# Performance work log

Hardware: AMD Instinct MI355X
Metric: run time of the kernel (lower is better)

## Reference

```python
import jax, jax.numpy as jnp
import numpy as np

D_MODEL = 1024
NUM_HEADS = 16
HEAD_DIM = D_MODEL // NUM_HEADS
SCALE = HEAD_DIM ** -0.5


def setup_inputs() -> dict:
    key = jax.random.key(0)
    ks = jax.random.split(key, 9)
    B, T, D = 4, 2048, D_MODEL
    s = 1.0 / np.sqrt(D)
    inp = {
        'x': jax.random.normal(ks[0], (B, T, D), dtype=jnp.float32),
        'Wq': jax.random.normal(ks[1], (D, D), dtype=jnp.float32) * s,
        'bq': jnp.zeros((D,), dtype=jnp.float32),
        'Wk': jax.random.normal(ks[2], (D, D), dtype=jnp.float32) * s,
        'bk': jnp.zeros((D,), dtype=jnp.float32),
        'Wv': jax.random.normal(ks[3], (D, D), dtype=jnp.float32) * s,
        'bv': jnp.zeros((D,), dtype=jnp.float32),
        'Wo': jax.random.normal(ks[4], (D, D), dtype=jnp.float32) * s,
        'bo': jnp.zeros((D,), dtype=jnp.float32),
    }
    return inp


def reference(x, Wq, bq, Wk, bk, Wv, bv, Wo, bo):
    B, T, D = x.shape
    H, hd = NUM_HEADS, HEAD_DIM
    # projections -> [B, H, T, hd]
    q = (x @ Wq + bq).reshape(B, T, H, hd).transpose(0, 2, 1, 3)
    k = (x @ Wk + bk).reshape(B, T, H, hd).transpose(0, 2, 1, 3)
    v = (x @ Wv + bv).reshape(B, T, H, hd).transpose(0, 2, 1, 3)
    # scores [B, H, T, T] with causal mask (triu above diagonal masked)
    scores = jnp.einsum('bhqd,bhkd->bhqk', q, k) * SCALE
    causal = jnp.triu(jnp.ones((T, T), dtype=bool), k=1)  # T_total == T
    scores = jnp.where(causal[None, None, :, :], -jnp.inf, scores)
    attn = jax.nn.softmax(scores, axis=-1)
    out = jnp.einsum('bhqk,bhkd->bhqd', attn, v)
    out = out.transpose(0, 2, 1, 3).reshape(B, T, D)
    return out @ Wo + bo
```

## Files before the change

### kernel.cpp

```cpp
#include <hip/hip_runtime.h>
#include <hip/hip_bf16.h>
#include <cmath>

#define TSEQ 2048
#define DMODEL 1024
#define NHEAD 16
#define HDIM 64
#define BATCH 4
#define MTOT (BATCH*TSEQ)

typedef __attribute__((ext_vector_type(8))) short bf16x8;
typedef __attribute__((ext_vector_type(4))) float f32x4;
typedef __attribute__((ext_vector_type(16))) float f32x16;
typedef unsigned short u16;
typedef unsigned int u32;
typedef __attribute__((ext_vector_type(2))) unsigned int u32x2;

#define QSCALE 0.18033688011112042f

__device__ __forceinline__ u16 f2bf(float f) {
    union { float f; unsigned u; } v; v.f = f;
    unsigned r = (v.u + 0x7fffu + ((v.u >> 16) & 1u)) >> 16;
    return (u16)r;
}

__device__ __forceinline__ u32 cvtpk(float a, float b) {
    u32 r;
    asm("v_cvt_pk_bf16_f32 %0, %1, %2" : "=v"(r) : "v"(a), "v"(b));
    return r;
}

#define GLOAD16(g, s) __builtin_amdgcn_global_load_lds( \
    (const __attribute__((address_space(1))) void*)(g), \
    (__attribute__((address_space(3))) void*)(s), 16, 0, 0)

__global__ __launch_bounds__(256) void cvt_x(const float* __restrict__ x,
                                             u16* __restrict__ xb) {
    int i = (blockIdx.x * 256 + threadIdx.x) * 4;
    float4 v = *(const float4*)(x + i);
    ushort4 o;
    o.x = f2bf(v.x); o.y = f2bf(v.y); o.z = f2bf(v.z); o.w = f2bf(v.w);
    *(ushort4*)(xb + i) = o;
}

__global__ __launch_bounds__(256) void wtrans(const float* __restrict__ W,
                                              u16* __restrict__ WT) {
    __shared__ float tile[64][65];
    int n0 = blockIdx.x * 64, k0 = blockIdx.y * 64;
    int t = threadIdx.x;
    int r = t >> 4;
    int c4 = (t & 15) * 4;
#pragma unroll
    for (int rr = 0; rr < 4; rr++) {
        int k = rr * 16 + r;
        float4 v = *(const float4*)(W + (size_t)(k0 + k) * DMODEL + n0 + c4);
        tile[k][c4 + 0] = v.x; tile[k][c4 + 1] = v.y;
        tile[k][c4 + 2] = v.z; tile[k][c4 + 3] = v.w;
    }
    __syncthreads();
#pragma unroll
    for (int rr = 0; rr < 4; rr++) {
        int n = rr * 16 + r;
        ushort4 o;
        o.x = f2bf(tile[c4 + 0][n]);
        o.y = f2bf(tile[c4 + 1][n]);
        o.z = f2bf(tile[c4 + 2][n]);
        o.w = f2bf(tile[c4 + 3][n]);
        *(ushort4*)(WT + (size_t)(n0 + n) * DMODEL + k0 + c4) = o;
    }
}

__global__ __launch_bounds__(256) void pack_bias(const float* __restrict__ bq,
                                                 const float* __restrict__ bk,
                                                 const float* __restrict__ bv,
                                                 float* __restrict__ bp) {
    int i = blockIdx.x * 256 + threadIdx.x;
    float v = (i < 1024) ? bq[i] * QSCALE : (i < 2048) ? bk[i - 1024] : bv[i - 2048];
    bp[i] = v;
}

template<int MODE>
__global__ __launch_bounds__(256) void gemm_bt(const u16* __restrict__ A,
                                               const u16* __restrict__ BT,
                                               const float* __restrict__ bias,
                                               u16* __restrict__ Qg,
                                               u16* __restrict__ Kg,
                                               u16* __restrict__ VTg,
                                               float* __restrict__ Fout,
                                               int K) {
    __shared__ __align__(16) u16 lA[2 * 4096];
    __shared__ __align__(16) u16 lB[2 * 4096];
    int nwg = gridDim.x * gridDim.y;
    int bid = blockIdx.y * gridDim.x + blockIdx.x;
    int cpx = nwg >> 3;
    int swz = (bid & 7) * cpx + (bid >> 3);
    int bx = swz % gridDim.x, by = swz / gridDim.x;
    int m0 = by * 128, n0 = bx * 128;
    int t = threadIdx.x, l = t & 63, w = t >> 6;
    int wr = w >> 1, wc = w & 1;
    int lg = l >> 4, lr = l & 15;
    f32x4 acc[4][4];
#pragma unroll
    for (int i = 0; i < 4; i++)
#pragma unroll
        for (int j = 0; j < 4; j++) acc[i][j] = (f32x4){0.f, 0.f, 0.f, 0.f};

    auto STAGE = [&](int kt, int nbuf) {
        int k0 = kt << 5;
#pragma unroll
        for (int s = 0; s < 2; ++s) {
            int cc = t + s * 256;
            int row = cc >> 2, ko = (cc & 3) * 8;
            GLOAD16(A  + (size_t)(m0 + row) * K + k0 + ko,
                    lA + nbuf * 4096 + (s * 256 + w * 64) * 8);
            GLOAD16(BT + (size_t)(n0 + row) * K + k0 + ko,
                    lB + nbuf * 4096 + (s * 256 + w * 64) * 8);
        }
    };

    STAGE(0, 0);
    asm volatile("s_waitcnt vmcnt(0)" ::: "memory");
    __syncthreads();
    int nb = 0;
    int KT = K >> 5;
    for (int kt = 0; kt < KT; ++kt) {
        if (kt + 1 < KT) STAGE(kt + 1, nb ^ 1);
        const u16* a_ = lA + nb * 4096;
        const u16* b_ = lB + nb * 4096;
        bf16x8 af[4], bfr[4];
#pragma unroll
        for (int i = 0; i < 4; i++) {
            af[i]  = *(const bf16x8*)(a_ + (wr * 64 + i * 16 + lr) * 32 + lg * 8);
            bfr[i] = *(const bf16x8*)(b_ + (wc * 64 + i * 16 + lr) * 32 + lg * 8);
        }
        __builtin_amdgcn_s_setprio(1);
#pragma unroll
        for (int mi = 0; mi < 4; mi++)
#pragma unroll
            for (int ni = 0; ni < 4; ni++)
                acc[mi][ni] = __builtin_amdgcn_mfma_f32_16x16x32_bf16(
                    af[mi], bfr[ni], acc[mi][ni], 0, 0, 0);
        __builtin_amdgcn_s_setprio(0);
        asm volatile("s_waitcnt vmcnt(0)" ::: "memory");
        __syncthreads();
        nb ^= 1;
    }

    if (MODE == 0) {
        int seg = n0 >> 10;
        float ss = (seg == 0) ? QSCALE : 1.0f;
        u16* outb = (seg == 0) ? Qg : (seg == 1) ? Kg : VTg;
#pragma unroll
        for (int mi = 0; mi < 4; mi++)
#pragma unroll
            for (int ni = 0; ni < 4; ni++) {
                int ng = n0 + wc * 64 + ni * 16 + lr;
                int ngl = ng & 1023;
                int h = ngl >> 6, d = ngl & 63;
                int mg0 = m0 + wr * 64 + mi * 16 + lg * 4;
                int bb = mg0 >> 11, tq0 = mg0 & 2047;
                float bsv = bias[ng];
                if (seg == 2) {
                    ushort4 o;
                    o.x = f2bf(acc[mi][ni][0] + bsv);
                    o.y = f2bf(acc[mi][ni][1] + bsv);
                    o.z = f2bf(acc[mi][ni][2] + bsv);
                    o.w = f2bf(acc[mi][ni][3] + bsv);
                    *(ushort4*)&VTg[(((size_t)(bb * NHEAD + h)) * HDIM + d) * TSEQ + tq0] = o;
                } else {
#pragma unroll
                    for (int r = 0; r < 4; r++) {
                        float v = acc[mi][ni][r] * ss + bsv;
                        outb[(((size_t)(bb * NHEAD + h)) * TSEQ + tq0 + r) * HDIM + d] = f2bf(v);
                    }
                }
            }
    } else {
#pragma unroll
        for (int mi = 0; mi < 4; mi++)
#pragma unroll
            for (int ni = 0; ni < 4; ni++) {
                int ng = n0 + wc * 64 + ni * 16 + lr;
                int mg0 = m0 + wr * 64 + mi * 16 + lg * 4;
                float bsv = bias[ng];
#pragma unroll
                for (int r = 0; r < 4; r++)
                    Fout[(size_t)(mg0 + r) * DMODEL + ng] = acc[mi][ni][r] + bsv;
            }
    }
}

__global__ __launch_bounds__(256) void attn(const u16* __restrict__ Qg,
                                            const u16* __restrict__ Kg,
                                            const u16* __restrict__ VTg,
                                            u16* __restrict__ Og) {
    __shared__ __align__(16) u16 sK[2 * 4096];
    __shared__ __align__(16) u16 sV[2 * 4096];
    const int bh = blockIdx.x;
    const int p  = blockIdx.y;
    const int tid = threadIdx.x;
    const int wv = tid >> 6;
    const int l  = tid & 63;
    const int ln = l & 31;
    const int hi = l >> 5;
    const int b = bh >> 4, h = bh & 15;

    auto STAGE = [&](int tt, int nbuf) {
        int kv0s = tt << 6;
#pragma unroll
        for (int s = 0; s < 2; ++s) {
            int cc = tid + s * 256;
            int row = cc >> 3, c = cc & 7;
            int csrc = c ^ (row & 7);
            GLOAD16(Kg + ((size_t)bh * TSEQ + kv0s + row) * HDIM + csrc * 8,
                    sK + nbuf * 4096 + (s * 256 + wv * 64) * 8);
            GLOAD16(VTg + ((size_t)bh * HDIM + row) * TSEQ + kv0s + csrc * 8,
                    sV + nbuf * 4096 + (s * 256 + wv * 64) * 8);
        }
    };

    for (int pass = 0; pass < 2; ++pass) {
        const int sidx = pass ? (15 - p) : p;
        const int qs = sidx << 7;
        const int NT = (qs >> 6) + 2;
        const int q0w = qs + wv * 32;
        const int qglob = q0w + ln;

        bf16x8 qf0, qf1, qf2, qf3;
        {
            const u16* qb = Qg + ((size_t)bh * TSEQ + qglob) * HDIM + hi * 8;
            qf0 = *(const bf16x8*)(qb);
            qf1 = *(const bf16x8*)(qb + 16);
            qf2 = *(const bf16x8*)(qb + 32);
            qf3 = *(const bf16x8*)(qb + 48);
        }
        float mrun = -INFINITY, lsum = 0.f;
        f32x16 accO0, accO1;
#pragma unroll
        for (int i = 0; i < 16; ++i) { accO0[i] = 0.f; accO1[i] = 0.f; }

        int nb = 0;
        STAGE(0, 0);
        asm volatile("s_waitcnt vmcnt(0)" ::: "memory");
        __syncthreads();

        for (int t = 0; t < NT; ++t) {
            if (t + 1 < NT) STAGE(t + 1, nb ^ 1);
            const int kv0 = t << 6;
            if (kv0 <= q0w + 31) {
                const u16* sKb = sK + nb * 4096;
                const u16* sVb = sV + nb * 4096;
                f32x16 sc0, sc1;
#pragma unroll
                for (int i = 0; i < 16; ++i) { sc0[i] = 0.f; sc1[i] = 0.f; }
                __builtin_amdgcn_s_setprio(1);
#pragma unroll
                for (int c = 0; c < 4; ++c) {
                    int u = ((c << 1) | hi) ^ (ln & 7);
                    bf16x8 kf0 = *(const bf16x8*)(sKb + ln * 64 + u * 8);
                    bf16x8 kf1 = *(const bf16x8*)(sKb + (32 + ln) * 64 + u * 8);
                    bf16x8 qq = (c == 0) ? qf0 : (c == 1) ? qf1 : (c == 2) ? qf2 : qf3;
                    sc0 = __builtin_amdgcn_mfma_f32_32x32x16_bf16(kf0, qq, sc0, 0, 0, 0);
                    sc1 = __builtin_amdgcn_mfma_f32_32x32x16_bf16(kf1, qq, sc1, 0, 0, 0);
                }
                __builtin_amdgcn_s_setprio(0);

                if (kv0 + 63 > q0w) {
                    const int qrel = qglob - kv0;
#pragma unroll
                    for (int r = 0; r < 16; ++r) {
                        int e0 = (r & 3) + 8 * (r >> 2) + 4 * hi;
                        if (e0 > qrel) sc0[r] = -INFINITY;
                        if (e0 + 32 > qrel) sc1[r] = -INFINITY;
                    }
                }

                float pmax = -INFINITY;
#pragma unroll
                for (int r = 0; r < 16; ++r) pmax = fmaxf(pmax, fmaxf(sc0[r], sc1[r]));
                pmax = fmaxf(pmax, __shfl_xor(pmax, 32, 64));
                const float nm = fmaxf(mrun, pmax);
                const float fc = exp2f(mrun - nm);
                mrun = nm;
                float ps = 0.f;
#pragma unroll
                for (int r = 0; r < 16; ++r) {
                    sc0[r] = exp2f(sc0[r] - nm);
                    sc1[r] = exp2f(sc1[r] - nm);
                    ps += sc0[r] + sc1[r];
                }
                ps += __shfl_xor(ps, 32, 64);
                lsum = lsum * fc + ps;
#pragma unroll
                for (int i = 0; i < 16; ++i) { accO0[i] *= fc; accO1[i] *= fc; }

                bf16x8 pf[4];
#pragma unroll
                for (int c = 0; c < 4; ++c) {
                    const int bb = (c & 1) * 8;
                    float s0, s1, s2, s3, s4, s5, s6, s7;
                    if (c < 2) {
                        s0 = sc0[bb + 0]; s1 = sc0[bb + 1]; s2 = sc0[bb + 2]; s3 = sc0[bb + 3];
                        s4 = sc0[bb + 4]; s5 = sc0[bb + 5]; s6 = sc0[bb + 6]; s7 = sc0[bb + 7];
                    } else {
                        s0 = sc1[bb + 0]; s1 = sc1[bb + 1]; s2 = sc1[bb + 2]; s3 = sc1[bb + 3];
                        s4 = sc1[bb + 4]; s5 = sc1[bb + 5]; s6 = sc1[bb + 6]; s7 = sc1[bb + 7];
                    }
                    u32 A  = cvtpk(s0, s1);
                    u32 A2 = cvtpk(s2, s3);
                    u32 Bp = cvtpk(s4, s5);
                    u32 B2 = cvtpk(s6, s7);
                    u32x2 r02 = __builtin_amdgcn_permlane32_swap(A, Bp, 0, 0);
                    u32x2 r13 = __builtin_amdgcn_permlane32_swap(A2, B2, 0, 0);
                    union { u32 w[4]; bf16x8 v; } pu;
                    pu.w[0] = r02[0]; pu.w[1] = r13[0];
                    pu.w[2] = r02[1]; pu.w[3] = r13[1];
                    pf[c] = pu.v;
                }

                __builtin_amdgcn_s_setprio(1);
#pragma unroll
                for (int c = 0; c < 4; ++c) {
                    int u = ((c << 1) | hi) ^ (ln & 7);
                    bf16x8 vf0 = *(const bf16x8*)(sVb + ln * 64 + u * 8);
                    bf16x8 vf1 = *(const bf16x8*)(sVb + (32 + ln) * 64 + u * 8);
                    accO0 = __builtin_amdgcn_mfma_f32_32x32x16_bf16(vf0, pf[c], accO0, 0, 0, 0);
                    accO1 = __builtin_amdgcn_mfma_f32_32x32x16_bf16(vf1, pf[c], accO1, 0, 0, 0);
                }
                __builtin_amdgcn_s_setprio(0);
            }
            asm volatile("s_waitcnt vmcnt(0)" ::: "memory");
            __syncthreads();
            nb ^= 1;
        }

        const float linv = 1.0f / lsum;
        u16* orow = Og + ((size_t)(b * TSEQ + qglob)) * DMODEL + h * HDIM;
#pragma unroll
        for (int a = 0; a < 4; ++a) {
            int d0 = 8 * a + 4 * hi;
            uint2 wo;
            wo.x = cvtpk(accO0[4 * a + 0] * linv, accO0[4 * a + 1] * linv);
            wo.y = cvtpk(accO0[4 * a + 2] * linv, accO0[4 * a + 3] * linv);
            *(uint2*)(orow + d0) = wo;
            wo.x = cvtpk(accO1[4 * a + 0] * linv, accO1[4 * a + 1] * linv);
            wo.y = cvtpk(accO1[4 * a + 2] * linv, accO1[4 * a + 3] * linv);
            *(uint2*)(orow + 32 + d0) = wo;
        }
    }
}

extern "C" void kernel_launch(void* const* d_in, const int* in_sizes, int n_in,
                              void* d_out, int out_size, void* d_ws, size_t ws_size,
                              hipStream_t stream) {
    const float* x  = (const float*)d_in[0];
    const float* Wq = (const float*)d_in[1];
    const float* bq = (const float*)d_in[2];
    const float* Wk = (const float*)d_in[3];
    const float* bk = (const float*)d_in[4];
    const float* Wv = (const float*)d_in[5];
    const float* bv = (const float*)d_in[6];
    const float* Wo = (const float*)d_in[7];
    const float* bo = (const float*)d_in[8];
    float* out = (float*)d_out;

    u16* ws  = (u16*)d_ws;
    u16* xb  = ws;
    u16* WqT = xb  + (size_t)MTOT * DMODEL;
    u16* WkT = WqT + (size_t)DMODEL * DMODEL;
    u16* WvT = WkT + (size_t)DMODEL * DMODEL;
    u16* WoT = WvT + (size_t)DMODEL * DMODEL;
    u16* Qg  = WoT + (size_t)DMODEL * DMODEL;
    u16* Kg  = Qg  + (size_t)MTOT * DMODEL;
    u16* VTg = Kg  + (size_t)MTOT * DMODEL;
    u16* Og  = VTg + (size_t)MTOT * DMODEL;
    float* biasP = (float*)(Og + (size_t)MTOT * DMODEL);

    cvt_x<<<(MTOT * DMODEL) / (256 * 4), 256, 0, stream>>>(x, xb);
    dim3 tg(16, 16);
    wtrans<<<tg, 256, 0, stream>>>(Wq, WqT);
    wtrans<<<tg, 256, 0, stream>>>(Wk, WkT);
    wtrans<<<tg, 256, 0, stream>>>(Wv, WvT);
    wtrans<<<tg, 256, 0, stream>>>(Wo, WoT);
    pack_bias<<<12, 256, 0, stream>>>(bq, bk, bv, biasP);

    gemm_bt<0><<<dim3(24, MTOT / 128), 256, 0, stream>>>(xb, WqT, biasP,
                                                         Qg, Kg, VTg, nullptr, DMODEL);

    attn<<<dim3(64, 8), 256, 0, stream>>>(Qg, Kg, VTg, Og);

    gemm_bt<3><<<dim3(8, MTOT / 128), 256, 0, stream>>>(Og, WoT, bo,
                                                        nullptr, nullptr, nullptr, out, DMODEL);
}
```

Measured before the change: 307.3 us.

## Triple-buffer GEMM and attention tiles; lazy softmax rescale with lane-swap reductions

```diff
diff --git a/kernel.cpp b/kernel.cpp
--- a/kernel.cpp
+++ b/kernel.cpp
@@ -28,6 +28,14 @@
     u32 r;
     asm("v_cvt_pk_bf16_f32 %0, %1, %2" : "=v"(r) : "v"(a), "v"(b));
     return r;
+}
+
+__device__ __forceinline__ float2 swap32(float x) {
+    union { float f; u32 u; } a; a.f = x;
+    u32x2 r = __builtin_amdgcn_permlane32_swap(a.u, a.u, 0, 0);
+    union { u32 u; float f; } p, q;
+    p.u = r[0]; q.u = r[1];
+    return make_float2(p.f, q.f);
 }
 
 #define GLOAD16(g, s) __builtin_amdgcn_global_load_lds( \
@@ -88,8 +96,7 @@
                                                u16* __restrict__ VTg,
                                                float* __restrict__ Fout,
                                                int K) {
-    __shared__ __align__(16) u16 lA[2 * 4096];
-    __shared__ __align__(16) u16 lB[2 * 4096];
+    __shared__ __align__(16) u16 lds[6 * 4096];
     int nwg = gridDim.x * gridDim.y;
     int bid = blockIdx.y * gridDim.x + blockIdx.x;
     int cpx = nwg >> 3;
@@ -112,21 +119,23 @@
             int cc = t + s * 256;
             int row = cc >> 2, ko = (cc & 3) * 8;
             GLOAD16(A  + (size_t)(m0 + row) * K + k0 + ko,
-                    lA + nbuf * 4096 + (s * 256 + w * 64) * 8);
+                    lds + nbuf * 4096 + (s * 256 + w * 64) * 8);
             GLOAD16(BT + (size_t)(n0 + row) * K + k0 + ko,
-                    lB + nbuf * 4096 + (s * 256 + w * 64) * 8);
+                    lds + 12288 + nbuf * 4096 + (s * 256 + w * 64) * 8);
         }
     };
 
+    const int KT = K >> 5;
     STAGE(0, 0);
-    asm volatile("s_waitcnt vmcnt(0)" ::: "memory");
+    STAGE(1, 1);
+    asm volatile("s_waitcnt vmcnt(4)" ::: "memory");
     __syncthreads();
-    int nb = 0;
-    int KT = K >> 5;
+    int cur = 0;
     for (int kt = 0; kt < KT; ++kt) {
-        if (kt + 1 < KT) STAGE(kt + 1, nb ^ 1);
-        const u16* a_ = lA + nb * 4096;
-        const u16* b_ = lB + nb * 4096;
+        int sb = cur + 2; if (sb >= 3) sb -= 3;
+        if (kt + 2 < KT) STAGE(kt + 2, sb);
+        const u16* a_ = lds + cur * 4096;
+        const u16* b_ = lds + 12288 + cur * 4096;
         bf16x8 af[4], bfr[4];
 #pragma unroll
         for (int i = 0; i < 4; i++) {
@@ -141,9 +150,10 @@
                 acc[mi][ni] = __builtin_amdgcn_mfma_f32_16x16x32_bf16(
                     af[mi], bfr[ni], acc[mi][ni], 0, 0, 0);
         __builtin_amdgcn_s_setprio(0);
-        asm volatile("s_waitcnt vmcnt(0)" ::: "memory");
+        if (kt + 2 < KT)      asm volatile("s_waitcnt vmcnt(4)" ::: "memory");
+        else if (kt + 1 < KT) asm volatile("s_waitcnt vmcnt(0)" ::: "memory");
         __syncthreads();
-        nb ^= 1;
+        cur = (cur == 2) ? 0 : cur + 1;
     }
 
     if (MODE == 0) {
@@ -194,8 +204,8 @@
                                             const u16* __restrict__ Kg,
                                             const u16* __restrict__ VTg,
                                             u16* __restrict__ Og) {
-    __shared__ __align__(16) u16 sK[2 * 4096];
-    __shared__ __align__(16) u16 sV[2 * 4096];
+    __shared__ __align__(16) u16 sK[3 * 4096];
+    __shared__ __align__(16) u16 sV[3 * 4096];
     const int bh = blockIdx.x;
     const int p  = blockIdx.y;
     const int tid = threadIdx.x;
@@ -239,17 +249,19 @@
 #pragma unroll
         for (int i = 0; i < 16; ++i) { accO0[i] = 0.f; accO1[i] = 0.f; }
 
-        int nb = 0;
         STAGE(0, 0);
-        asm volatile("s_waitcnt vmcnt(0)" ::: "memory");
+        STAGE(1, 1);
+        asm volatile("s_waitcnt vmcnt(4)" ::: "memory");
         __syncthreads();
+        int cur = 0;
 
         for (int t = 0; t < NT; ++t) {
-            if (t + 1 < NT) STAGE(t + 1, nb ^ 1);
+            int sb = cur + 2; if (sb >= 3) sb -= 3;
+            if (t + 2 < NT) STAGE(t + 2, sb);
             const int kv0 = t << 6;
             if (kv0 <= q0w + 31) {
-                const u16* sKb = sK + nb * 4096;
-                const u16* sVb = sV + nb * 4096;
+                const u16* sKb = sK + cur * 4096;
+                const u16* sVb = sV + cur * 4096;
                 f32x16 sc0, sc1;
 #pragma unroll
                 for (int i = 0; i < 16; ++i) { sc0[i] = 0.f; sc1[i] = 0.f; }
@@ -275,24 +287,49 @@
                     }
                 }
 
-                float pmax = -INFINITY;
-#pragma unroll
-                for (int r = 0; r < 16; ++r) pmax = fmaxf(pmax, fmaxf(sc0[r], sc1[r]));
-                pmax = fmaxf(pmax, __shfl_xor(pmax, 32, 64));
-                const float nm = fmaxf(mrun, pmax);
-                const float fc = exp2f(mrun - nm);
-                mrun = nm;
-                float ps = 0.f;
+                float mx[8];
+#pragma unroll
+                for (int r = 0; r < 8; ++r)
+                    mx[r] = fmaxf(fmaxf(sc0[r], sc0[r + 8]), fmaxf(sc1[r], sc1[r + 8]));
+                mx[0] = fmaxf(mx[0], mx[4]); mx[1] = fmaxf(mx[1], mx[5]);
+                mx[2] = fmaxf(mx[2], mx[6]); mx[3] = fmaxf(mx[3], mx[7]);
+                mx[0] = fmaxf(mx[0], mx[2]); mx[1] = fmaxf(mx[1], mx[3]);
+                float pmax;
+                {
+                    float2 sw = swap32(fmaxf(mx[0], mx[1]));
+                    pmax = fmaxf(sw.x, sw.y);
+                }
+
+                unsigned long long need = __ballot(pmax > mrun + 8.0f);
+                float fc = 1.0f;
+                if (need) {
+                    float nm = fmaxf(mrun, pmax);
+                    fc = exp2f(mrun - nm);
+                    mrun = nm;
+                }
 #pragma unroll
                 for (int r = 0; r < 16; ++r) {
-                    sc0[r] = exp2f(sc0[r] - nm);
-                    sc1[r] = exp2f(sc1[r] - nm);
-                    ps += sc0[r] + sc1[r];
-                }
-                ps += __shfl_xor(ps, 32, 64);
-                lsum = lsum * fc + ps;
-#pragma unroll
-                for (int i = 0; i < 16; ++i) { accO0[i] *= fc; accO1[i] *= fc; }
+                    sc0[r] = exp2f(sc0[r] - mrun);
+                    sc1[r] = exp2f(sc1[r] - mrun);
+                }
+                float sm[8];
+#pragma unroll
+                for (int r = 0; r < 8; ++r)
+                    sm[r] = (sc0[r] + sc0[r + 8]) + (sc1[r] + sc1[r + 8]);
+                sm[0] += sm[4]; sm[1] += sm[5]; sm[2] += sm[6]; sm[3] += sm[7];
+                sm[0] += sm[2]; sm[1] += sm[3];
+                float ps;
+                {
+                    float2 sw = swap32(sm[0] + sm[1]);
+                    ps = sw.x + sw.y;
+                }
+                if (need) {
+                    lsum = lsum * fc + ps;
+#pragma unroll
+                    for (int i = 0; i < 16; ++i) { accO0[i] *= fc; accO1[i] *= fc; }
+                } else {
+                    lsum += ps;
+                }
 
                 bf16x8 pf[4];
 #pragma unroll
@@ -329,9 +366,10 @@
                 }
                 __builtin_amdgcn_s_setprio(0);
             }
-            asm volatile("s_waitcnt vmcnt(0)" ::: "memory");
+            if (t + 2 < NT)      asm volatile("s_waitcnt vmcnt(4)" ::: "memory");
+            else if (t + 1 < NT) asm volatile("s_waitcnt vmcnt(0)" ::: "memory");
             __syncthreads();
-            nb ^= 1;
+            cur = (cur == 2) ? 0 : cur + 1;
         }
 
         const float linv = 1.0f / lsum;
```

Result: slower. 330.3 us (+7.5%).
